# Kernel optimization log

Hardware: AMD Instinct MI355X
Metric: run time of the kernel (lower is better)

## Reference

```python
import jax, jax.numpy as jnp
import numpy as np

B, S, P, K, D, H = 16384, 512, 1024, 8, 64, 128


def setup_inputs() -> dict:
    key = jax.random.key(0)
    ks = jax.random.split(key, 8)
    return {
        "skl_pfc": jax.random.normal(ks[0], (B, S), dtype=jnp.float32),
        "tensor_mask": jnp.ones((B, P), dtype=jnp.float32),
        "skl_emd": jax.random.normal(ks[1], (S, D), dtype=jnp.float32),
        "plm_emd": jax.random.normal(ks[2], (P, D), dtype=jnp.float32),
        "W": jax.random.normal(ks[3], (H, D), dtype=jnp.float32) * 0.05,
        "U": jax.random.normal(ks[4], (H, D), dtype=jnp.float32) * 0.05,
        "v_T": jax.random.normal(ks[5], (1, H), dtype=jnp.float32) * 0.05,
        "group_idx": jax.random.randint(ks[6], (P, K), 0, S, dtype=jnp.int64),
    }


def reference(skl_pfc, tensor_mask, skl_emd, plm_emd, W, U, v_T, group_idx):
    # Per problem p: align = v_T @ tanh(W @ plm_p + U @ skl_emd[S_p].T)
    proj_p = plm_emd @ W.T                       # [P, H]
    proj_s = (skl_emd @ U.T)[group_idx]          # [P, K, H] gather of projected skills
    scores = jnp.einsum("h,pkh->pk", v_T[0], jnp.tanh(proj_p[:, None, :] + proj_s))  # [P, K]
    att = jax.nn.softmax(scores, axis=-1)        # softmax over each problem's skill group
    # Weighted sum of gathered skill proficiencies -> per-problem proficiency
    out = jnp.einsum("bpk,pk->bp", skl_pfc[:, group_idx], att)  # [B, P]
    return out * tensor_mask
```

## Files before the change

kernel.cpp:

```cpp
#include <hip/hip_runtime.h>
#include <cmath>

#define B_ 16384
#define S_ 512
#define P_ 1024
#define K_ 8
#define D_ 64
#define H_ 128
#define BT 8
#define PADU 4

typedef float f32x2 __attribute__((ext_vector_type(2)));

static __device__ __forceinline__ unsigned int rne16(float f) {
  unsigned int u = __float_as_uint(f);
  return (u + 0x7fffu + ((u >> 16) & 1u)) >> 16;
}
static __device__ __forceinline__ float bflo(unsigned int u) { return __uint_as_float(u << 16); }
static __device__ __forceinline__ float bfhi(unsigned int u) { return __uint_as_float(u & 0xffff0000u); }

__global__ __launch_bounds__(128) void proj_skl_kernel(
    const float* __restrict__ skl_emd, const float* __restrict__ U,
    float* __restrict__ sklproj) {
  __shared__ float row[D_];
  const int s = blockIdx.x, h = threadIdx.x;
  if (h < D_) row[h] = skl_emd[s * D_ + h];
  __syncthreads();
  float acc = 0.f;
#pragma unroll
  for (int d = 0; d < D_; d++) acc += row[d] * U[h * D_ + d];
  sklproj[s * H_ + h] = acc;
}

__global__ __launch_bounds__(128) void att_kernel(
    const float* __restrict__ plm_emd, const float* __restrict__ W,
    const float* __restrict__ vT, const float* __restrict__ sklproj,
    const int* __restrict__ gidx, float* __restrict__ att) {
  __shared__ float prow[D_];
  __shared__ float red[2][K_];
  const int p = blockIdx.x, h = threadIdx.x;
  if (h < D_) prow[h] = plm_emd[p * D_ + h];
  __syncthreads();
  float pp = 0.f;
#pragma unroll
  for (int d = 0; d < D_; d++) pp += prow[d] * W[h * D_ + d];
  const float v = vT[h];
  int g[K_];
#pragma unroll
  for (int k = 0; k < K_; k++) g[k] = gidx[p * K_ + k];
  float partial[K_];
#pragma unroll
  for (int k = 0; k < K_; k++) partial[k] = v * tanhf(pp + sklproj[g[k] * H_ + h]);
#pragma unroll
  for (int off = 32; off >= 1; off >>= 1)
#pragma unroll
    for (int k = 0; k < K_; k++) partial[k] += __shfl_down(partial[k], off, 64);
  const int wave = h >> 6, lane = h & 63;
  if (lane == 0)
#pragma unroll
    for (int k = 0; k < K_; k++) red[wave][k] = partial[k];
  __syncthreads();
  if (h == 0) {
    float s[K_], m = -1e30f;
#pragma unroll
    for (int k = 0; k < K_; k++) { s[k] = red[0][k] + red[1][k]; m = fmaxf(m, s[k]); }
    float denom = 0.f;
#pragma unroll
    for (int k = 0; k < K_; k++) { s[k] = expf(s[k] - m); denom += s[k]; }
    const float inv = 1.f / denom;
#pragma unroll
    for (int k = 0; k < K_; k++) att[p * K_ + k] = s[k] * inv;
  }
}

__global__ __launch_bounds__(256) void out_kernel(
    const float* __restrict__ skl_pfc, const float* __restrict__ mask,
    const float* __restrict__ att, const int* __restrict__ gidx,
    float* __restrict__ out) {
  __shared__ __align__(16) unsigned int rowsT[S_][PADU];
  const int t = threadIdx.x;
  const int b0 = blockIdx.x * BT;

#pragma unroll
  for (int i = 0; i < S_ / 256; i++) {
    const int s = t + i * 256;
    unsigned int pk[PADU];
#pragma unroll
    for (int q = 0; q < PADU; q++) {
      const float f0 = __builtin_nontemporal_load(&skl_pfc[(size_t)(b0 + 2 * q) * S_ + s]);
      const float f1 = __builtin_nontemporal_load(&skl_pfc[(size_t)(b0 + 2 * q + 1) * S_ + s]);
      pk[q] = rne16(f0) | (rne16(f1) << 16);
    }
    *(uint4*)&rowsT[s][0] = make_uint4(pk[0], pk[1], pk[2], pk[3]);
  }
  __syncthreads();

#pragma unroll
  for (int j = 0; j < 2; j++) {
    const int p = 2 * t + j * 512;
    const float4* ap = (const float4*)(att + (size_t)p * K_);
    const int4* gp = (const int4*)(gidx + (size_t)p * K_);
    const float4 a0 = ap[0], a1 = ap[1], a2 = ap[2], a3 = ap[3];
    const int4 g0 = gp[0], g1 = gp[1], g2 = gp[2], g3 = gp[3];
    const float av0[K_] = {a0.x, a0.y, a0.z, a0.w, a1.x, a1.y, a1.z, a1.w};
    const int gv0[K_] = {g0.x, g0.y, g0.z, g0.w, g1.x, g1.y, g1.z, g1.w};
    const float av1[K_] = {a2.x, a2.y, a2.z, a2.w, a3.x, a3.y, a3.z, a3.w};
    const int gv1[K_] = {g2.x, g2.y, g2.z, g2.w, g3.x, g3.y, g3.z, g3.w};

    f32x2 m2[BT];
#pragma unroll
    for (int bb = 0; bb < BT; bb++)
      m2[bb] = __builtin_nontemporal_load(
          (const f32x2*)&mask[(size_t)(b0 + bb) * P_ + p]);

    float acc0[BT] = {0.f, 0.f, 0.f, 0.f, 0.f, 0.f, 0.f, 0.f};
    float acc1[BT] = {0.f, 0.f, 0.f, 0.f, 0.f, 0.f, 0.f, 0.f};
#pragma unroll
    for (int k = 0; k < K_; k++) {
      const uint4 q0 = *(const uint4*)&rowsT[gv0[k]][0];
      const float a = av0[k];
      acc0[0] += bflo(q0.x) * a; acc0[1] += bfhi(q0.x) * a;
      acc0[2] += bflo(q0.y) * a; acc0[3] += bfhi(q0.y) * a;
      acc0[4] += bflo(q0.z) * a; acc0[5] += bfhi(q0.z) * a;
      acc0[6] += bflo(q0.w) * a; acc0[7] += bfhi(q0.w) * a;
    }
#pragma unroll
    for (int k = 0; k < K_; k++) {
      const uint4 q1 = *(const uint4*)&rowsT[gv1[k]][0];
      const float a = av1[k];
      acc1[0] += bflo(q1.x) * a; acc1[1] += bfhi(q1.x) * a;
      acc1[2] += bflo(q1.y) * a; acc1[3] += bfhi(q1.y) * a;
      acc1[4] += bflo(q1.z) * a; acc1[5] += bfhi(q1.z) * a;
      acc1[6] += bflo(q1.w) * a; acc1[7] += bfhi(q1.w) * a;
    }
#pragma unroll
    for (int bb = 0; bb < BT; bb++) {
      f32x2 o;
      o.x = acc0[bb] * m2[bb].x;
      o.y = acc1[bb] * m2[bb].y;
      __builtin_nontemporal_store(o, (f32x2*)&out[(size_t)(b0 + bb) * P_ + p]);
    }
  }
}

extern "C" void kernel_launch(void* const* d_in, const int* in_sizes, int n_in,
                              void* d_out, int out_size, void* d_ws, size_t ws_size,
                              hipStream_t stream) {
  const float* skl_pfc = (const float*)d_in[0];
  const float* mask    = (const float*)d_in[1];
  const float* skl_emd = (const float*)d_in[2];
  const float* plm_emd = (const float*)d_in[3];
  const float* W       = (const float*)d_in[4];
  const float* U       = (const float*)d_in[5];
  const float* vT      = (const float*)d_in[6];
  const int*   gidx    = (const int*)d_in[7];
  float* out = (float*)d_out;

  float* sklproj = (float*)d_ws;
  float* att     = sklproj + S_ * H_;

  proj_skl_kernel<<<S_, 128, 0, stream>>>(skl_emd, U, sklproj);
  att_kernel<<<P_, 128, 0, stream>>>(plm_emd, W, vT, sklproj, gidx, att);
  out_kernel<<<B_ / BT, 256, 0, stream>>>(skl_pfc, mask, att, gidx, out);
}
```

Measured before the change: 170.8 us.

## Make out_kernel persistent with double-buffered LDS and register prefetch

The output kernel now launches a fixed grid of 1024 blocks that loop over batch tiles instead of one block per tile. Each block loads its attention weights and indices into registers once, and prefetches the next tile's skl_pfc rows into registers while computing the current tile out of a double-buffered LDS array. This hides global load latency and amortises the att/gidx loads across tiles. The cost is higher register pressure and more LDS, which may lower occupancy.

```diff
diff --git a/kernel.cpp b/kernel.cpp
--- a/kernel.cpp
+++ b/kernel.cpp
@@ -9,6 +9,8 @@
 #define H_ 128
 #define BT 8
 #define PADU 4
+#define GRID_C 1024
+#define NT (B_ / BT)
 
 typedef float f32x2 __attribute__((ext_vector_type(2)));
 
@@ -77,69 +79,115 @@
     const float* __restrict__ skl_pfc, const float* __restrict__ mask,
     const float* __restrict__ att, const int* __restrict__ gidx,
     float* __restrict__ out) {
-  __shared__ __align__(16) unsigned int rowsT[S_][PADU];
+  __shared__ __align__(16) unsigned int rowsT[2][S_][PADU];
   const int t = threadIdx.x;
-  const int b0 = blockIdx.x * BT;
-
-#pragma unroll
-  for (int i = 0; i < S_ / 256; i++) {
-    const int s = t + i * 256;
-    unsigned int pk[PADU];
-#pragma unroll
-    for (int q = 0; q < PADU; q++) {
-      const float f0 = __builtin_nontemporal_load(&skl_pfc[(size_t)(b0 + 2 * q) * S_ + s]);
-      const float f1 = __builtin_nontemporal_load(&skl_pfc[(size_t)(b0 + 2 * q + 1) * S_ + s]);
-      pk[q] = rne16(f0) | (rne16(f1) << 16);
+
+  float aA[K_], aB[K_], aC[K_], aD[K_];
+  int gA[K_], gB[K_], gC[K_], gD[K_];
+  {
+    const int pj0 = 2 * t, pj1 = 2 * t + 512;
+    const float4* ap0 = (const float4*)(att + (size_t)pj0 * K_);
+    const int4* gp0 = (const int4*)(gidx + (size_t)pj0 * K_);
+    const float4* ap1 = (const float4*)(att + (size_t)pj1 * K_);
+    const int4* gp1 = (const int4*)(gidx + (size_t)pj1 * K_);
+    const float4 a0 = ap0[0], a1 = ap0[1], a2 = ap0[2], a3 = ap0[3];
+    const int4 g0 = gp0[0], g1 = gp0[1], g2 = gp0[2], g3 = gp0[3];
+    const float4 a4 = ap1[0], a5 = ap1[1], a6 = ap1[2], a7 = ap1[3];
+    const int4 g4 = gp1[0], g5 = gp1[1], g6 = gp1[2], g7 = gp1[3];
+    aA[0]=a0.x; aA[1]=a0.y; aA[2]=a0.z; aA[3]=a0.w; aA[4]=a1.x; aA[5]=a1.y; aA[6]=a1.z; aA[7]=a1.w;
+    aB[0]=a2.x; aB[1]=a2.y; aB[2]=a2.z; aB[3]=a2.w; aB[4]=a3.x; aB[5]=a3.y; aB[6]=a3.z; aB[7]=a3.w;
+    aC[0]=a4.x; aC[1]=a4.y; aC[2]=a4.z; aC[3]=a4.w; aC[4]=a5.x; aC[5]=a5.y; aC[6]=a5.z; aC[7]=a5.w;
+    aD[0]=a6.x; aD[1]=a6.y; aD[2]=a6.z; aD[3]=a6.w; aD[4]=a7.x; aD[5]=a7.y; aD[6]=a7.z; aD[7]=a7.w;
+    gA[0]=g0.x; gA[1]=g0.y; gA[2]=g0.z; gA[3]=g0.w; gA[4]=g1.x; gA[5]=g1.y; gA[6]=g1.z; gA[7]=g1.w;
+    gB[0]=g2.x; gB[1]=g2.y; gB[2]=g2.z; gB[3]=g2.w; gB[4]=g3.x; gB[5]=g3.y; gB[6]=g3.z; gB[7]=g3.w;
+    gC[0]=g4.x; gC[1]=g4.y; gC[2]=g4.z; gC[3]=g4.w; gC[4]=g5.x; gC[5]=g5.y; gC[6]=g5.z; gC[7]=g5.w;
+    gD[0]=g6.x; gD[1]=g6.y; gD[2]=g6.z; gD[3]=g6.w; gD[4]=g7.x; gD[5]=g7.y; gD[6]=g7.z; gD[7]=g7.w;
+  }
+
+  float st[16];
+
+  auto PREFETCH = [&](int tile) {
+    const int b0 = tile * BT;
+#pragma unroll
+    for (int i = 0; i < 2; i++) {
+      const int s = t + i * 256;
+#pragma unroll
+      for (int b = 0; b < 8; b++)
+        st[i * 8 + b] =
+            __builtin_nontemporal_load(&skl_pfc[(size_t)(b0 + b) * S_ + s]);
     }
-    *(uint4*)&rowsT[s][0] = make_uint4(pk[0], pk[1], pk[2], pk[3]);
-  }
-  __syncthreads();
-
-#pragma unroll
-  for (int j = 0; j < 2; j++) {
-    const int p = 2 * t + j * 512;
-    const float4* ap = (const float4*)(att + (size_t)p * K_);
-    const int4* gp = (const int4*)(gidx + (size_t)p * K_);
-    const float4 a0 = ap[0], a1 = ap[1], a2 = ap[2], a3 = ap[3];
-    const int4 g0 = gp[0], g1 = gp[1], g2 = gp[2], g3 = gp[3];
-    const float av0[K_] = {a0.x, a0.y, a0.z, a0.w, a1.x, a1.y, a1.z, a1.w};
-    const int gv0[K_] = {g0.x, g0.y, g0.z, g0.w, g1.x, g1.y, g1.z, g1.w};
-    const float av1[K_] = {a2.x, a2.y, a2.z, a2.w, a3.x, a3.y, a3.z, a3.w};
-    const int gv1[K_] = {g2.x, g2.y, g2.z, g2.w, g3.x, g3.y, g3.z, g3.w};
-
-    f32x2 m2[BT];
-#pragma unroll
-    for (int bb = 0; bb < BT; bb++)
-      m2[bb] = __builtin_nontemporal_load(
-          (const f32x2*)&mask[(size_t)(b0 + bb) * P_ + p]);
-
-    float acc0[BT] = {0.f, 0.f, 0.f, 0.f, 0.f, 0.f, 0.f, 0.f};
-    float acc1[BT] = {0.f, 0.f, 0.f, 0.f, 0.f, 0.f, 0.f, 0.f};
-#pragma unroll
-    for (int k = 0; k < K_; k++) {
-      const uint4 q0 = *(const uint4*)&rowsT[gv0[k]][0];
-      const float a = av0[k];
-      acc0[0] += bflo(q0.x) * a; acc0[1] += bfhi(q0.x) * a;
-      acc0[2] += bflo(q0.y) * a; acc0[3] += bfhi(q0.y) * a;
-      acc0[4] += bflo(q0.z) * a; acc0[5] += bfhi(q0.z) * a;
-      acc0[6] += bflo(q0.w) * a; acc0[7] += bfhi(q0.w) * a;
+  };
+
+  auto PACK = [&](int buf) {
+#pragma unroll
+    for (int i = 0; i < 2; i++) {
+      const int s = t + i * 256;
+      unsigned int pk[PADU];
+#pragma unroll
+      for (int q = 0; q < PADU; q++)
+        pk[q] = rne16(st[i * 8 + 2 * q]) | (rne16(st[i * 8 + 2 * q + 1]) << 16);
+      *(uint4*)&rowsT[buf][s][0] = make_uint4(pk[0], pk[1], pk[2], pk[3]);
     }
-#pragma unroll
-    for (int k = 0; k < K_; k++) {
-      const uint4 q1 = *(const uint4*)&rowsT[gv1[k]][0];
-      const float a = av1[k];
-      acc1[0] += bflo(q1.x) * a; acc1[1] += bfhi(q1.x) * a;
-      acc1[2] += bflo(q1.y) * a; acc1[3] += bfhi(q1.y) * a;
-      acc1[4] += bflo(q1.z) * a; acc1[5] += bfhi(q1.z) * a;
-      acc1[6] += bflo(q1.w) * a; acc1[7] += bfhi(q1.w) * a;
+  };
+
+  auto COMPUTE = [&](int tile, int buf) {
+    const int b0 = tile * BT;
+#pragma unroll
+    for (int j = 0; j < 2; j++) {
+      const int p = 2 * t + j * 512;
+      const float* av0 = (j == 0) ? aA : aC;
+      const float* av1 = (j == 0) ? aB : aD;
+      const int* gv0 = (j == 0) ? gA : gC;
+      const int* gv1 = (j == 0) ? gB : gD;
+
+      f32x2 m2[BT];
+#pragma unroll
+      for (int bb = 0; bb < BT; bb++)
+        m2[bb] = __builtin_nontemporal_load(
+            (const f32x2*)&mask[(size_t)(b0 + bb) * P_ + p]);
+
+      float acc0[BT] = {0.f, 0.f, 0.f, 0.f, 0.f, 0.f, 0.f, 0.f};
+      float acc1[BT] = {0.f, 0.f, 0.f, 0.f, 0.f, 0.f, 0.f, 0.f};
+#pragma unroll
+      for (int k = 0; k < K_; k++) {
+        const uint4 q0 = *(const uint4*)&rowsT[buf][gv0[k]][0];
+        const float a = av0[k];
+        acc0[0] += bflo(q0.x) * a; acc0[1] += bfhi(q0.x) * a;
+        acc0[2] += bflo(q0.y) * a; acc0[3] += bfhi(q0.y) * a;
+        acc0[4] += bflo(q0.z) * a; acc0[5] += bfhi(q0.z) * a;
+        acc0[6] += bflo(q0.w) * a; acc0[7] += bfhi(q0.w) * a;
+      }
+#pragma unroll
+      for (int k = 0; k < K_; k++) {
+        const uint4 q1 = *(const uint4*)&rowsT[buf][gv1[k]][0];
+        const float a = av1[k];
+        acc1[0] += bflo(q1.x) * a; acc1[1] += bfhi(q1.x) * a;
+        acc1[2] += bflo(q1.y) * a; acc1[3] += bfhi(q1.y) * a;
+        acc1[4] += bflo(q1.z) * a; acc1[5] += bfhi(q1.z) * a;
+        acc1[6] += bflo(q1.w) * a; acc1[7] += bfhi(q1.w) * a;
+      }
+#pragma unroll
+      for (int bb = 0; bb < BT; bb++) {
+        f32x2 o;
+        o.x = acc0[bb] * m2[bb].x;
+        o.y = acc1[bb] * m2[bb].y;
+        __builtin_nontemporal_store(o, (f32x2*)&out[(size_t)(b0 + bb) * P_ + p]);
+      }
     }
-#pragma unroll
-    for (int bb = 0; bb < BT; bb++) {
-      f32x2 o;
-      o.x = acc0[bb] * m2[bb].x;
-      o.y = acc1[bb] * m2[bb].y;
-      __builtin_nontemporal_store(o, (f32x2*)&out[(size_t)(b0 + bb) * P_ + p]);
-    }
+  };
+
+  int tile = blockIdx.x;
+  int buf = 0;
+  PREFETCH(tile);
+  for (;;) {
+    PACK(buf);
+    __syncthreads();
+    const int next = tile + GRID_C;
+    if (next < NT) PREFETCH(next);
+    COMPUTE(tile, buf);
+    if (next >= NT) break;
+    tile = next;
+    buf ^= 1;
   }
 }
 
@@ -161,5 +209,5 @@
 
   proj_skl_kernel<<<S_, 128, 0, stream>>>(skl_emd, U, sklproj);
   att_kernel<<<P_, 128, 0, stream>>>(plm_emd, W, vT, sklproj, gidx, att);
-  out_kernel<<<B_ / BT, 256, 0, stream>>>(skl_pfc, mask, att, gidx, out);
-}
+  out_kernel<<<GRID_C, 256, 0, stream>>>(skl_pfc, mask, att, gidx, out);
+}
```

Result: faster. 167.2 us (-2.1%).

## Recast gather-weighted sum as dense fp16 MFMA GEMM with scattered attention matrix

Applied to the files above, without the earlier changes.

Builds a dense [P,S] fp16 attention matrix by zeroing a workspace and scattering each problem's softmax weights, merging duplicate indices. The output becomes an MFMA GEMM of skl_pfc (converted to fp16 on load) against that matrix, with the mask applied in the epilogue. This swaps the gather-based out_kernel for matrix-core work and adds two small kernels plus a 1 MB matrix. The dense GEMM does 64x the arithmetic of the sparse form and writes output with uncoalesced scalar stores. The projection kernels also switch to float4 weight loads.

```diff
diff --git a/kernel.cpp b/kernel.cpp
--- a/kernel.cpp
+++ b/kernel.cpp
@@ -7,17 +7,10 @@
 #define K_ 8
 #define D_ 64
 #define H_ 128
-#define BT 8
-#define PADU 4
 
 typedef float f32x2 __attribute__((ext_vector_type(2)));
-
-static __device__ __forceinline__ unsigned int rne16(float f) {
-  unsigned int u = __float_as_uint(f);
-  return (u + 0x7fffu + ((u >> 16) & 1u)) >> 16;
-}
-static __device__ __forceinline__ float bflo(unsigned int u) { return __uint_as_float(u << 16); }
-static __device__ __forceinline__ float bfhi(unsigned int u) { return __uint_as_float(u & 0xffff0000u); }
+typedef float f32x4 __attribute__((ext_vector_type(4)));
+typedef _Float16 half8 __attribute__((ext_vector_type(8)));
 
 __global__ __launch_bounds__(128) void proj_skl_kernel(
     const float* __restrict__ skl_emd, const float* __restrict__ U,
@@ -26,9 +19,16 @@
   const int s = blockIdx.x, h = threadIdx.x;
   if (h < D_) row[h] = skl_emd[s * D_ + h];
   __syncthreads();
+  const float4* __restrict__ Urow = (const float4*)(U + (size_t)h * D_);
   float acc = 0.f;
 #pragma unroll
-  for (int d = 0; d < D_; d++) acc += row[d] * U[h * D_ + d];
+  for (int i = 0; i < D_ / 4; i++) {
+    const float4 u = Urow[i];
+    acc += row[4 * i] * u.x;
+    acc += row[4 * i + 1] * u.y;
+    acc += row[4 * i + 2] * u.z;
+    acc += row[4 * i + 3] * u.w;
+  }
   sklproj[s * H_ + h] = acc;
 }
 
@@ -41,9 +41,16 @@
   const int p = blockIdx.x, h = threadIdx.x;
   if (h < D_) prow[h] = plm_emd[p * D_ + h];
   __syncthreads();
+  const float4* __restrict__ Wrow = (const float4*)(W + (size_t)h * D_);
   float pp = 0.f;
 #pragma unroll
-  for (int d = 0; d < D_; d++) pp += prow[d] * W[h * D_ + d];
+  for (int i = 0; i < D_ / 4; i++) {
+    const float4 w = Wrow[i];
+    pp += prow[4 * i] * w.x;
+    pp += prow[4 * i + 1] * w.y;
+    pp += prow[4 * i + 2] * w.z;
+    pp += prow[4 * i + 3] * w.w;
+  }
   const float v = vT[h];
   int g[K_];
 #pragma unroll
@@ -73,72 +80,109 @@
   }
 }
 
-__global__ __launch_bounds__(256) void out_kernel(
-    const float* __restrict__ skl_pfc, const float* __restrict__ mask,
+__global__ __launch_bounds__(256) void zero_AT_kernel(_Float16* __restrict__ AT) {
+  const int i = blockIdx.x * 256 + threadIdx.x;
+  ((uint4*)AT)[i] = make_uint4(0u, 0u, 0u, 0u);
+}
+
+__global__ __launch_bounds__(256) void build_AT_kernel(
     const float* __restrict__ att, const int* __restrict__ gidx,
-    float* __restrict__ out) {
-  __shared__ __align__(16) unsigned int rowsT[S_][PADU];
+    _Float16* __restrict__ AT) {
+  const int p = blockIdx.x * 256 + threadIdx.x;
+  const float4* ap = (const float4*)(att + (size_t)p * K_);
+  const int4* gp = (const int4*)(gidx + (size_t)p * K_);
+  const float4 a0 = ap[0], a1 = ap[1];
+  const int4 g0 = gp[0], g1 = gp[1];
+  float a[K_] = {a0.x, a0.y, a0.z, a0.w, a1.x, a1.y, a1.z, a1.w};
+  int g[K_] = {g0.x, g0.y, g0.z, g0.w, g1.x, g1.y, g1.z, g1.w};
+#pragma unroll
+  for (int k = 1; k < K_; k++)
+#pragma unroll
+    for (int j = 0; j < K_; j++) {
+      if (j >= k) break;
+      if (g[j] == g[k]) { a[j] += a[k]; g[k] = -1; break; }
+    }
+#pragma unroll
+  for (int k = 0; k < K_; k++)
+    if (g[k] >= 0) AT[(size_t)p * S_ + g[k]] = (_Float16)a[k];
+}
+
+__global__ __launch_bounds__(256) void gemm_kernel(
+    const float* __restrict__ pfc, const float* __restrict__ mask,
+    const _Float16* __restrict__ AT, float* __restrict__ out) {
+  __shared__ _Float16 pA[128][72];
+  __shared__ _Float16 pB[128][72];
   const int t = threadIdx.x;
-  const int b0 = blockIdx.x * BT;
-
-#pragma unroll
-  for (int i = 0; i < S_ / 256; i++) {
-    const int s = t + i * 256;
-    unsigned int pk[PADU];
-#pragma unroll
-    for (int q = 0; q < PADU; q++) {
-      const float f0 = __builtin_nontemporal_load(&skl_pfc[(size_t)(b0 + 2 * q) * S_ + s]);
-      const float f1 = __builtin_nontemporal_load(&skl_pfc[(size_t)(b0 + 2 * q + 1) * S_ + s]);
-      pk[q] = rne16(f0) | (rne16(f1) << 16);
-    }
-    *(uint4*)&rowsT[s][0] = make_uint4(pk[0], pk[1], pk[2], pk[3]);
-  }
-  __syncthreads();
-
-#pragma unroll
-  for (int j = 0; j < 2; j++) {
-    const int p = 2 * t + j * 512;
-    const float4* ap = (const float4*)(att + (size_t)p * K_);
-    const int4* gp = (const int4*)(gidx + (size_t)p * K_);
-    const float4 a0 = ap[0], a1 = ap[1], a2 = ap[2], a3 = ap[3];
-    const int4 g0 = gp[0], g1 = gp[1], g2 = gp[2], g3 = gp[3];
-    const float av0[K_] = {a0.x, a0.y, a0.z, a0.w, a1.x, a1.y, a1.z, a1.w};
-    const int gv0[K_] = {g0.x, g0.y, g0.z, g0.w, g1.x, g1.y, g1.z, g1.w};
-    const float av1[K_] = {a2.x, a2.y, a2.z, a2.w, a3.x, a3.y, a3.z, a3.w};
-    const int gv1[K_] = {g2.x, g2.y, g2.z, g2.w, g3.x, g3.y, g3.z, g3.w};
-
-    f32x2 m2[BT];
-#pragma unroll
-    for (int bb = 0; bb < BT; bb++)
-      m2[bb] = __builtin_nontemporal_load(
-          (const f32x2*)&mask[(size_t)(b0 + bb) * P_ + p]);
-
-    float acc0[BT] = {0.f, 0.f, 0.f, 0.f, 0.f, 0.f, 0.f, 0.f};
-    float acc1[BT] = {0.f, 0.f, 0.f, 0.f, 0.f, 0.f, 0.f, 0.f};
-#pragma unroll
-    for (int k = 0; k < K_; k++) {
-      const uint4 q0 = *(const uint4*)&rowsT[gv0[k]][0];
-      const float a = av0[k];
-      acc0[0] += bflo(q0.x) * a; acc0[1] += bfhi(q0.x) * a;
-      acc0[2] += bflo(q0.y) * a; acc0[3] += bfhi(q0.y) * a;
-      acc0[4] += bflo(q0.z) * a; acc0[5] += bfhi(q0.z) * a;
-      acc0[6] += bflo(q0.w) * a; acc0[7] += bfhi(q0.w) * a;
-    }
-#pragma unroll
-    for (int k = 0; k < K_; k++) {
-      const uint4 q1 = *(const uint4*)&rowsT[gv1[k]][0];
-      const float a = av1[k];
-      acc1[0] += bflo(q1.x) * a; acc1[1] += bfhi(q1.x) * a;
-      acc1[2] += bflo(q1.y) * a; acc1[3] += bfhi(q1.y) * a;
-      acc1[4] += bflo(q1.z) * a; acc1[5] += bfhi(q1.z) * a;
-      acc1[6] += bflo(q1.w) * a; acc1[7] += bfhi(q1.w) * a;
-    }
-#pragma unroll
-    for (int bb = 0; bb < BT; bb++) {
-      f32x2 o;
-      o.x = acc0[bb] * m2[bb].x;
-      o.y = acc1[bb] * m2[bb].y;
-      __builtin_nontemporal_store(o, (f32x2*)&out[(size_t)(b0 + bb) * P_ + p]);
+  const int d = blockIdx.x;
+  const int xx = d & 7, yy = d >> 3;
+  const int mq = xx + 8 * (yy >> 3);
+  const int nj = yy & 7;
+  const int b0 = mq * 128, p0 = nj * 128;
+  const int l = t & 63, wid = t >> 6;
+  const int wm = (wid >> 1) * 64, wn = (wid & 1) * 64;
+  const int lr = l & 15, lq = l >> 4;
+
+  f32x4 acc[4][4];
+#pragma unroll
+  for (int i = 0; i < 4; i++)
+#pragma unroll
+    for (int j = 0; j < 4; j++) acc[i][j] = (f32x4){0.f, 0.f, 0.f, 0.f};
+
+  for (int step = 0; step < 8; ++step) {
+    const int s0 = step * 64;
+    __syncthreads();
+    {
+      const int r = t >> 2, c16 = (t & 3) * 16;
+#pragma unroll
+      for (int pass = 0; pass < 2; ++pass) {
+        const int row = r + 64 * pass;
+        const float4* src = (const float4*)&pfc[(size_t)(b0 + row) * S_ + s0 + c16];
+        const float4 v0 = src[0], v1 = src[1], v2 = src[2], v3 = src[3];
+        half8 h0, h1;
+        h0[0] = (_Float16)v0.x; h0[1] = (_Float16)v0.y; h0[2] = (_Float16)v0.z; h0[3] = (_Float16)v0.w;
+        h0[4] = (_Float16)v1.x; h0[5] = (_Float16)v1.y; h0[6] = (_Float16)v1.z; h0[7] = (_Float16)v1.w;
+        h1[0] = (_Float16)v2.x; h1[1] = (_Float16)v2.y; h1[2] = (_Float16)v2.z; h1[3] = (_Float16)v2.w;
+        h1[4] = (_Float16)v3.x; h1[5] = (_Float16)v3.y; h1[6] = (_Float16)v3.z; h1[7] = (_Float16)v3.w;
+        *(half8*)&pA[row][c16] = h0;
+        *(half8*)&pA[row][c16 + 8] = h1;
+      }
+    }
+    {
+      const int pr = t >> 1, c32 = (t & 1) * 32;
+      const uint4* src = (const uint4*)&AT[(size_t)(p0 + pr) * S_ + s0 + c32];
+#pragma unroll
+      for (int i = 0; i < 4; ++i) *(uint4*)&pB[pr][c32 + 8 * i] = src[i];
+    }
+    __syncthreads();
+#pragma unroll
+    for (int kk = 0; kk < 64; kk += 32) {
+      half8 aF[4], bF[4];
+#pragma unroll
+      for (int fm = 0; fm < 4; ++fm)
+        aF[fm] = *(const half8*)&pA[wm + fm * 16 + lr][kk + lq * 8];
+#pragma unroll
+      for (int fn = 0; fn < 4; ++fn)
+        bF[fn] = *(const half8*)&pB[wn + fn * 16 + lr][kk + lq * 8];
+#pragma unroll
+      for (int fm = 0; fm < 4; ++fm)
+#pragma unroll
+        for (int fn = 0; fn < 4; ++fn)
+          acc[fm][fn] = __builtin_amdgcn_mfma_f32_16x16x32_f16(
+              aF[fm], bF[fn], acc[fm][fn], 0, 0, 0);
+    }
+  }
+
+#pragma unroll
+  for (int fm = 0; fm < 4; ++fm) {
+#pragma unroll
+    for (int j = 0; j < 4; ++j) {
+      const int row = b0 + wm + fm * 16 + lq * 4 + j;
+#pragma unroll
+      for (int fn = 0; fn < 4; ++fn) {
+        const int col = p0 + wn + fn * 16 + lr;
+        const size_t idx = (size_t)row * P_ + col;
+        out[idx] = acc[fm][fn][j] * mask[idx];
+      }
     }
   }
 }
@@ -158,8 +202,11 @@
 
   float* sklproj = (float*)d_ws;
   float* att     = sklproj + S_ * H_;
+  _Float16* AT   = (_Float16*)(att + P_ * K_);
 
   proj_skl_kernel<<<S_, 128, 0, stream>>>(skl_emd, U, sklproj);
   att_kernel<<<P_, 128, 0, stream>>>(plm_emd, W, vT, sklproj, gidx, att);
-  out_kernel<<<B_ / BT, 256, 0, stream>>>(skl_pfc, mask, att, gidx, out);
-}
+  zero_AT_kernel<<<256, 256, 0, stream>>>(AT);
+  build_AT_kernel<<<P_ / 256, 256, 0, stream>>>(att, gidx, AT);
+  gemm_kernel<<<1024, 256, 0, stream>>>(skl_pfc, mask, AT, out);
+}
```

Result: slower. 197.8 us (+15.9%).
